# Performance work log

Hardware: AMD Instinct MI355X
Metric: run time of the kernel (lower is better)

## Reference

```python
import jax, jax.numpy as jnp
import numpy as np

TOP_K = 2
SCALING = 32.0 / 16.0  # lora_alpha / r

N, D, O = 4096, 4096, 4096   # tokens, in_features, out_features
E, H, R_RANK = 8, 3, 16      # experts, B-heads per expert, lora rank
W_SCALE = 0.02               # keep logits in a sane range


def setup_inputs() -> dict:
    key = jax.random.key(0)
    ks = jax.random.split(key, 6)
    return {
        "x": jax.random.normal(ks[0], (N, D), jnp.float32),
        "base_W": jax.random.normal(ks[1], (D, O), jnp.float32) * W_SCALE,
        "router_W": jax.random.normal(ks[2], (E, D), jnp.float32) * W_SCALE,
        "A": jax.random.normal(ks[3], (E, D, R_RANK), jnp.float32) * W_SCALE,
        "B": jax.random.normal(ks[4], (E, H, R_RANK, O), jnp.float32) * W_SCALE,
        "R": jax.random.normal(ks[5], (E, D, H), jnp.float32) * W_SCALE,
    }


def reference(x, base_W, router_W, A, B, R):
    # Base dense layer
    base = x @ base_W                                   # [N, O]
    # Expert router: softmax over experts, top-k gate renormalized
    probs = jax.nn.softmax(x @ router_W.T, axis=-1)     # [N, E]
    topv, topi = jax.lax.top_k(probs, TOP_K)            # [N, k]
    topv = topv / topv.sum(-1, keepdims=True)
    n_idx = jnp.arange(x.shape[0])[:, None]
    gate = jnp.zeros_like(probs).at[n_idx, topi].set(topv)  # dense [N, E] gate, 0 off top-k
    # Shared lora_A per expert
    a = jnp.einsum('nd,edr->ner', x, A)                 # [N, E, r]
    # Per-expert head router over lora_B heads
    head_w = jax.nn.softmax(jnp.einsum('nd,edh->neh', x, R), axis=-1)  # [N, E, H]
    # Head-weighted B projections, combined with expert gates
    delta = jnp.einsum('ner,neh,ehro,ne->no', a, head_w, B, gate)      # [N, O]
    return base + SCALING * delta
```

## Files before the change

kernel.cpp:

```cpp
#include <hip/hip_runtime.h>
#include <hip/hip_bf16.h>
#include <math.h>

typedef __bf16 bf16_t;
typedef __bf16 bf16x4_t __attribute__((ext_vector_type(4)));
typedef __bf16 bf16x8_t __attribute__((ext_vector_type(8)));
typedef float  f32x4_t  __attribute__((ext_vector_type(4)));

#define N_TOK 4096
#define D_IN  4096
#define O_OUT 4096
#define NEXP  8
#define NHEAD 3
#define RANK  16
#define KC2   384
#define PCOLS 256
#define NKZ   8
#define SCALING_F 2.0f


__device__ __forceinline__ void transpose_tile(const float* __restrict__ src,
                                               bf16_t* __restrict__ dst,
                                               int Rr, int Cc, int r0, int c0,
                                               float (*tile)[65]) {
  int q  = threadIdx.x & 15;
  int r4 = threadIdx.x >> 4;
  #pragma unroll
  for (int g = 0; g < 4; ++g) {
    int r = r4 + g * 16;
    float4 v = *(const float4*)(src + (size_t)(r0 + r) * Cc + c0 + q * 4);
    tile[r][q * 4 + 0] = v.x; tile[r][q * 4 + 1] = v.y;
    tile[r][q * 4 + 2] = v.z; tile[r][q * 4 + 3] = v.w;
  }
  __syncthreads();
  int j  = threadIdx.x & 7;
  int cc = threadIdx.x >> 3;
  #pragma unroll
  for (int h = 0; h < 2; ++h) {
    int c = cc + h * 32;
    bf16x8_t o;
    #pragma unroll
    for (int i = 0; i < 8; ++i) o[i] = (bf16_t)tile[j * 8 + i][c];
    *(bf16x8_t*)(dst + (size_t)(c0 + c) * Rr + r0 + j * 8) = o;
  }
}

__global__ __launch_bounds__(256) void prep_kernel(const float* __restrict__ x,
                                                   const float* __restrict__ base_W,
                                                   const float* __restrict__ rw,
                                                   const float* __restrict__ A,
                                                   const float* __restrict__ B,
                                                   const float* __restrict__ Rm,
                                                   bf16_t* __restrict__ xb,
                                                   bf16_t* __restrict__ WbT,
                                                   bf16_t* __restrict__ BbT,
                                                   bf16_t* __restrict__ PabT,
                                                   int* __restrict__ gidx,
                                                   float* __restrict__ gwv) {
  __shared__ float tile[64][65];
  int b = blockIdx.x;
  if (b < 4096) {
    transpose_tile(base_W, WbT, 4096, 4096, (b & 63) * 64, (b >> 6) * 64, tile);
  } else if (b < 5120) {
    int lane = threadIdx.x & 63;
    int wv = threadIdx.x >> 6;
    int n = (b - 4096) * 4 + wv;
    const float4* xv = (const float4*)(x + (size_t)n * D_IN);
    bf16x4_t* xo = (bf16x4_t*)(xb + (size_t)n * D_IN);
    float acc[NEXP] = {0, 0, 0, 0, 0, 0, 0, 0};
    for (int d = lane; d < D_IN / 4; d += 64) {
      float4 xx = xv[d];
      bf16x4_t ob = { (bf16_t)xx.x, (bf16_t)xx.y, (bf16_t)xx.z, (bf16_t)xx.w };
      xo[d] = ob;
      #pragma unroll
      for (int e = 0; e < NEXP; ++e) {
        float4 ww = ((const float4*)(rw + (size_t)e * D_IN))[d];
        acc[e] += xx.x * ww.x + xx.y * ww.y + xx.z * ww.z + xx.w * ww.w;
      }
    }
    #pragma unroll
    for (int e = 0; e < NEXP; ++e) {
      float v = acc[e];
      #pragma unroll
      for (int o = 32; o > 0; o >>= 1) v += __shfl_down(v, o);
      acc[e] = v;
    }
    if (lane == 0) {
      int i0 = 0; float l0 = acc[0];
      #pragma unroll
      for (int e = 1; e < NEXP; ++e) if (acc[e] > l0) { l0 = acc[e]; i0 = e; }
      int i1 = -1; float l1 = -3.4e38f;
      #pragma unroll
      for (int e = 0; e < NEXP; ++e) if (e != i0 && acc[e] > l1) { l1 = acc[e]; i1 = e; }
      float w0 = 1.f / (1.f + expf(l1 - l0));
      gidx[2 * n] = i0; gidx[2 * n + 1] = i1;
      gwv[2 * n] = w0;  gwv[2 * n + 1] = 1.f - w0;
    }
  } else if (b < 5504) {
    int t = b - 5120;
    transpose_tile(B, BbT, KC2, 4096, (t % 6) * 64, (t / 6) * 64, tile);
  } else {
    int c = b - 5504;
    for (int d = threadIdx.x; d < D_IN; d += 256) {
      float v = 0.f;
      if (c < 128) {
        int e = c >> 4, r = c & 15;
        v = A[((size_t)e * D_IN + d) * RANK + r];
      } else if (c < 152) {
        int qq = c - 128; int e = qq / 3, h = qq - 3 * e;
        v = Rm[((size_t)e * D_IN + d) * NHEAD + h];
      }
      PabT[(size_t)c * D_IN + d] = (bf16_t)v;
    }
  }
}

__global__ void gating_kernel(const float* __restrict__ projP, const int* __restrict__ gidx,
                              const float* __restrict__ gwv, bf16_t* __restrict__ C2b) {
  int n = blockIdx.x;
  int c = threadIdx.x;
  int e = c / 48;
  int h = (c % 48) / 16;
  int r = c & 15;
  int i0 = gidx[2 * n], i1 = gidx[2 * n + 1];
  float g = (e == i0) ? gwv[2 * n] : (e == i1) ? gwv[2 * n + 1] : 0.f;
  float val = 0.f;
  if (g != 0.f) {
    const float* p0 = projP + (size_t)n * PCOLS;
    const size_t S = (size_t)N_TOK * PCOLS;
    float h0 = 0.f, h1 = 0.f, h2 = 0.f, av = 0.f;
    #pragma unroll
    for (int z = 0; z < NKZ; ++z) {
      const float* pz = p0 + (size_t)z * S;
      h0 += pz[128 + e * 3 + 0];
      h1 += pz[128 + e * 3 + 1];
      h2 += pz[128 + e * 3 + 2];
      av += pz[e * 16 + r];
    }
    float mx = fmaxf(h0, fmaxf(h1, h2));
    float e0 = expf(h0 - mx), e1 = expf(h1 - mx), e2 = expf(h2 - mx);
    float hw = (h == 0 ? e0 : h == 1 ? e1 : e2) / (e0 + e1 + e2);
    val = SCALING_F * g * hw * av;
  }
  C2b[(size_t)n * KC2 + c] = (bf16_t)val;
}

__device__ __forceinline__ void run_kloop(f32x4_t (&acc)[4][4], bf16_t* sA, bf16_t* sB,
                                          const bf16_t* __restrict__ Ab, int lda,
                                          const bf16_t* __restrict__ Bb, int ldb, int K) {
  const int tid = threadIdx.x;
  const int lane = tid & 63;
  const int w = tid >> 6;
  const int wm = (w >> 1) * 64;
  const int wn = (w & 1) * 64;
  const int qd = lane >> 4;
  const int ln = lane & 15;
  const int sw = ln & 7;

  size_t offA[4], offB[4];
  int lo[4];
  #pragma unroll
  for (int t = 0; t < 4; ++t) {
    int c = tid + t * 256;
    int m = c >> 3, kc = (c & 7) ^ (m & 7);
    offA[t] = (size_t)m * lda + kc * 8;
    offB[t] = (size_t)m * ldb + kc * 8;
    lo[t] = c * 8;
  }
  int rowA[4], rowB[4];
  #pragma unroll
  for (int i = 0; i < 4; ++i) {
    rowA[i] = (wm + i * 16 + ln) * 64;
    rowB[i] = (wn + i * 16 + ln) * 64;
  }

  for (int k0 = 0; k0 < K; k0 += 64) {
    __syncthreads();
    #pragma unroll
    for (int t = 0; t < 4; ++t)
      __builtin_amdgcn_global_load_lds(
          (const __attribute__((address_space(1))) void*)(Ab + k0 + offA[t]),
          (__attribute__((address_space(3))) void*)(sA + lo[t]), 16, 0, 0);
    #pragma unroll
    for (int t = 0; t < 4; ++t)
      __builtin_amdgcn_global_load_lds(
          (const __attribute__((address_space(1))) void*)(Bb + k0 + offB[t]),
          (__attribute__((address_space(3))) void*)(sB + lo[t]), 16, 0, 0);
    __syncthreads();
    #pragma unroll
    for (int s = 0; s < 2; ++s) {
      bf16x8_t af[4], bfr[4];
      int kx = ((s * 4 + qd) ^ sw) * 8;
      #pragma unroll
      for (int i = 0; i < 4; ++i) af[i]  = *(const bf16x8_t*)(sA + rowA[i] + kx);
      #pragma unroll
      for (int i = 0; i < 4; ++i) bfr[i] = *(const bf16x8_t*)(sB + rowB[i] + kx);
      #pragma unroll
      for (int i = 0; i < 4; ++i)
        #pragma unroll
        for (int j = 0; j < 4; ++j)
          acc[i][j] = __builtin_amdgcn_mfma_f32_16x16x32_bf16(af[i], bfr[j], acc[i][j], 0, 0, 0);
    }
  }
}

__global__ __launch_bounds__(256) void gemm_proj_kernel(const bf16_t* __restrict__ xb,
                                                        const bf16_t* __restrict__ PabT,
                                                        float* __restrict__ projP) {
  __shared__ bf16_t sA[128 * 64];
  __shared__ bf16_t sB[128 * 64];
  int bm = blockIdx.x, bn = blockIdx.y, kz = blockIdx.z;
  f32x4_t acc[4][4] = {};
  run_kloop(acc, sA, sB,
            xb + (size_t)bm * 128 * D_IN + kz * 512, D_IN,
            PabT + (size_t)bn * 128 * D_IN + kz * 512, D_IN, 512);
  const int lane = threadIdx.x & 63, w = threadIdx.x >> 6;
  const int wm = (w >> 1) * 64, wn = (w & 1) * 64, qd = lane >> 4, ln = lane & 15;
  float* Cb = projP + (size_t)kz * N_TOK * PCOLS + (size_t)bm * 128 * PCOLS + bn * 128;
  #pragma unroll
  for (int i = 0; i < 4; ++i)
    #pragma unroll
    for (int j = 0; j < 4; ++j) {
      int col = wn + j * 16 + ln;
      #pragma unroll
      for (int rg = 0; rg < 4; ++rg) {
        int row = wm + i * 16 + qd * 4 + rg;
        Cb[(size_t)row * PCOLS + col] = acc[i][j][rg];
      }
    }
}


__device__ __forceinline__ void stage1(const bf16_t* __restrict__ G, int k0,
                                       bf16_t* lbase, size_t g, int tid) {
  __builtin_amdgcn_global_load_lds(
      (const __attribute__((address_space(1))) void*)(G + g + k0),
      (__attribute__((address_space(3))) void*)(lbase + tid * 8), 16, 0, 0);
}

template <int N>
__device__ __forceinline__ void vm_wait() {
  if constexpr (N == 6)      asm volatile("s_waitcnt vmcnt(6)" ::: "memory");
  else if constexpr (N == 4) asm volatile("s_waitcnt vmcnt(4)" ::: "memory");
  else if constexpr (N == 2) asm volatile("s_waitcnt vmcnt(2)" ::: "memory");
  else if constexpr (N == 0) asm volatile("s_waitcnt vmcnt(0)" ::: "memory");
}

template <int SC, bool STAGE, int VMN>
__device__ __forceinline__ void tbodyS(f32x4_t (&acc)[4][4], bf16_t* sring,
                                       const bf16_t* __restrict__ Ag,
                                       const bf16_t* __restrict__ Bg, int k3,
                                       size_t gA, size_t gB, int aoff, int boff, int tid) {
  constexpr int SS = (SC + 3) & 3;
  if constexpr (STAGE) {
    stage1(Ag, k3, sring + SS * 16384, gA, tid);
    stage1(Bg, k3, sring + SS * 16384 + 8192, gB, tid);
  }
  vm_wait<VMN>();
  __builtin_amdgcn_s_barrier();
  const bf16_t* pA = sring + SC * 16384 + aoff;
  const bf16_t* pB = sring + SC * 16384 + 8192 + boff;
  bf16x8_t af[4], bv[4];
  #pragma unroll
  for (int nj = 0; nj < 4; ++nj) bv[nj] = *(const bf16x8_t*)(pB + nj * 512);
  #pragma unroll
  for (int mi = 0; mi < 4; ++mi) af[mi] = *(const bf16x8_t*)(pA + mi * 512);
  __builtin_amdgcn_s_setprio(1);
  #pragma unroll
  for (int mi = 0; mi < 4; ++mi)
    #pragma unroll
    for (int nj = 0; nj < 4; ++nj)
      acc[mi][nj] = __builtin_amdgcn_mfma_f32_16x16x32_bf16(af[mi], bv[nj], acc[mi][nj], 0, 0, 0);
  __builtin_amdgcn_s_setprio(0);
  __builtin_amdgcn_sched_barrier(0);
  __builtin_amdgcn_s_barrier();
}

template <int K>
__device__ __forceinline__ void kloopS(f32x4_t (&acc)[4][4], bf16_t* sring,
                                       const bf16_t* __restrict__ A, int lda,
                                       const bf16_t* __restrict__ B, int ldb,
                                       int tid, int aoff, int boff) {
  constexpr int T = K / 32;
  static_assert((T & 3) == 0, "T must be multiple of 4");
  const int s = tid, r = s >> 2, c = (s & 3) ^ ((r >> 1) & 3);
  const size_t gA = (size_t)r * lda + c * 8;
  const size_t gB = (size_t)r * ldb + c * 8;

  #pragma unroll
  for (int t = 0; t < 3; ++t) {
    stage1(A, t * 32, sring + t * 16384, gA, tid);
    stage1(B, t * 32, sring + t * 16384 + 8192, gB, tid);
  }
  constexpr int TM = T - 3;
  int t = 0;
  for (; t + 3 < TM; t += 4) {
    tbodyS<0,true,6>(acc, sring, A, B, (t+3)*32, gA, gB, aoff, boff, tid);
    tbodyS<1,true,6>(acc, sring, A, B, (t+4)*32, gA, gB, aoff, boff, tid);
    tbodyS<2,true,6>(acc, sring, A, B, (t+5)*32, gA, gB, aoff, boff, tid);
    tbodyS<3,true,6>(acc, sring, A, B, (t+6)*32, gA, gB, aoff, boff, tid);
  }
  tbodyS<0,true,6>(acc, sring, A, B, (t+3)*32, gA, gB, aoff, boff, tid);
  tbodyS<1,false,4>(acc, sring, A, B, 0, gA, gB, aoff, boff, tid);
  tbodyS<2,false,2>(acc, sring, A, B, 0, gA, gB, aoff, boff, tid);
  tbodyS<3,false,0>(acc, sring, A, B, 0, gA, gB, aoff, boff, tid);
}

__global__ __launch_bounds__(1024, 1) void gemm_fused256(const bf16_t* __restrict__ xb,
                                                         const bf16_t* __restrict__ WbT,
                                                         const bf16_t* __restrict__ C2b,
                                                         const bf16_t* __restrict__ BbT,
                                                         float* __restrict__ out) {
  __shared__ __align__(16) bf16_t sring[4 * 16384];
  const int tid = threadIdx.x;
  const int lane = tid & 63;
  const int w = tid >> 6;
  const int wm = w >> 2;
  const int wn = w & 3;
  const int qd = lane >> 4;
  const int ln = lane & 15;
  const int swz8 = ((qd ^ ((ln >> 1) & 3)) << 3);

  int b = blockIdx.x;
  int sw = (b & 7) * 32 + (b >> 3);
  int bm = sw >> 4, bn = sw & 15;

  const int aoff = (wm * 64 + ln) * 32 + swz8;
  const int boff = (wn * 64 + ln) * 32 + swz8;

  f32x4_t acc[4][4] = {};

  kloopS<D_IN>(acc, sring, xb  + (size_t)bm * 256 * D_IN, D_IN,
                           WbT + (size_t)bn * 256 * D_IN, D_IN, tid, aoff, boff);
  kloopS<KC2>(acc, sring, C2b + (size_t)bm * 256 * KC2,  KC2,
                          BbT + (size_t)bn * 256 * KC2,  KC2,  tid, aoff, boff);

  float* Cb = out + (size_t)(bm * 256 + wm * 64) * O_OUT + bn * 256 + wn * 64;
  #pragma unroll
  for (int mi = 0; mi < 4; ++mi)
    #pragma unroll
    for (int nj = 0; nj < 4; ++nj)
      #pragma unroll
      for (int rg = 0; rg < 4; ++rg)
        Cb[(size_t)(mi * 16 + qd * 4 + rg) * O_OUT + nj * 16 + ln] = acc[mi][nj][rg];
}

extern "C" void kernel_launch(void* const* d_in, const int* in_sizes, int n_in,
                              void* d_out, int out_size, void* d_ws, size_t ws_size,
                              hipStream_t stream) {
  const float* x       = (const float*)d_in[0];
  const float* base_W  = (const float*)d_in[1];
  const float* routerW = (const float*)d_in[2];
  const float* A       = (const float*)d_in[3];
  const float* B       = (const float*)d_in[4];
  const float* Rm      = (const float*)d_in[5];
  float* out = (float*)d_out;
  char* ws = (char*)d_ws;

  bf16_t* xb   = (bf16_t*)(ws);
  bf16_t* WbT  = (bf16_t*)(ws + 33554432);
  bf16_t* PabT = (bf16_t*)(ws + 67108864);
  bf16_t* BbT  = (bf16_t*)(ws + 69206016);
  bf16_t* C2b  = (bf16_t*)(ws + 72351744);
  int*    gidx = (int*)   (ws + 75497472);
  float*  gwv  = (float*) (ws + 75530240);
  float*  projP = out;

  prep_kernel<<<5760, 256, 0, stream>>>(x, base_W, routerW, A, B, Rm,
                                        xb, WbT, BbT, PabT, gidx, gwv);
  gemm_proj_kernel<<<dim3(32, 2, NKZ), 256, 0, stream>>>(xb, PabT, projP);
  gating_kernel<<<4096, 384, 0, stream>>>(projP, gidx, gwv, C2b);
  gemm_fused256<<<dim3(256), 1024, 0, stream>>>(xb, WbT, C2b, BbT, out);
}
```

Before: 360.5 us.

## Shrink fused GEMM tile to 128x256 with double-buffered LDS and more blocks

The main fused GEMM moves from 256x256 tiles with 1024 threads and a 4-deep LDS ring to 128x256 tiles with 512 threads, a 2-stage double buffer, and 512 blocks. Launch bounds now allow several blocks per CU, so latency can be hidden across blocks instead of by deep prefetch within one block. Each thread now issues three async global-to-LDS loads per k-step. The trade is less operand reuse per tile and more global traffic for the B matrix, and the shallower prefetch could expose memory latency.

```diff
diff --git a/kernel.cpp b/kernel.cpp
--- a/kernel.cpp
+++ b/kernel.cpp
@@ -231,35 +231,39 @@
 }
 
 
-__device__ __forceinline__ void stage1(const bf16_t* __restrict__ G, int k0,
-                                       bf16_t* lbase, size_t g, int tid) {
+__device__ __forceinline__ void stageH(const bf16_t* __restrict__ Ag,
+                                       const bf16_t* __restrict__ Bg, int k0,
+                                       bf16_t* slot, size_t gA, size_t gB0, size_t gB1,
+                                       int tid) {
   __builtin_amdgcn_global_load_lds(
-      (const __attribute__((address_space(1))) void*)(G + g + k0),
-      (__attribute__((address_space(3))) void*)(lbase + tid * 8), 16, 0, 0);
+      (const __attribute__((address_space(1))) void*)(Ag + gA + k0),
+      (__attribute__((address_space(3))) void*)(slot + tid * 8), 16, 0, 0);
+  __builtin_amdgcn_global_load_lds(
+      (const __attribute__((address_space(1))) void*)(Bg + gB0 + k0),
+      (__attribute__((address_space(3))) void*)(slot + 4096 + tid * 8), 16, 0, 0);
+  __builtin_amdgcn_global_load_lds(
+      (const __attribute__((address_space(1))) void*)(Bg + gB1 + k0),
+      (__attribute__((address_space(3))) void*)(slot + 8192 + tid * 8), 16, 0, 0);
 }
 
 template <int N>
 __device__ __forceinline__ void vm_wait() {
-  if constexpr (N == 6)      asm volatile("s_waitcnt vmcnt(6)" ::: "memory");
-  else if constexpr (N == 4) asm volatile("s_waitcnt vmcnt(4)" ::: "memory");
-  else if constexpr (N == 2) asm volatile("s_waitcnt vmcnt(2)" ::: "memory");
+  if constexpr (N == 3)      asm volatile("s_waitcnt vmcnt(3)" ::: "memory");
   else if constexpr (N == 0) asm volatile("s_waitcnt vmcnt(0)" ::: "memory");
 }
 
 template <int SC, bool STAGE, int VMN>
-__device__ __forceinline__ void tbodyS(f32x4_t (&acc)[4][4], bf16_t* sring,
+__device__ __forceinline__ void tbodyH(f32x4_t (&acc)[4][4], bf16_t* sring,
                                        const bf16_t* __restrict__ Ag,
-                                       const bf16_t* __restrict__ Bg, int k3,
-                                       size_t gA, size_t gB, int aoff, int boff, int tid) {
-  constexpr int SS = (SC + 3) & 3;
-  if constexpr (STAGE) {
-    stage1(Ag, k3, sring + SS * 16384, gA, tid);
-    stage1(Bg, k3, sring + SS * 16384 + 8192, gB, tid);
-  }
+                                       const bf16_t* __restrict__ Bg, int k1,
+                                       size_t gA, size_t gB0, size_t gB1,
+                                       int aoff, int boff, int tid) {
+  if constexpr (STAGE)
+    stageH(Ag, Bg, k1, sring + (SC ^ 1) * 12288, gA, gB0, gB1, tid);
   vm_wait<VMN>();
   __builtin_amdgcn_s_barrier();
-  const bf16_t* pA = sring + SC * 16384 + aoff;
-  const bf16_t* pB = sring + SC * 16384 + 8192 + boff;
+  const bf16_t* pA = sring + SC * 12288 + aoff;
+  const bf16_t* pB = sring + SC * 12288 + 4096 + boff;
   bf16x8_t af[4], bv[4];
   #pragma unroll
   for (int nj = 0; nj < 4; ++nj) bv[nj] = *(const bf16x8_t*)(pB + nj * 512);
@@ -277,41 +281,35 @@
 }
 
 template <int K>
-__device__ __forceinline__ void kloopS(f32x4_t (&acc)[4][4], bf16_t* sring,
+__device__ __forceinline__ void kloopH(f32x4_t (&acc)[4][4], bf16_t* sring,
                                        const bf16_t* __restrict__ A, int lda,
                                        const bf16_t* __restrict__ B, int ldb,
                                        int tid, int aoff, int boff) {
   constexpr int T = K / 32;
-  static_assert((T & 3) == 0, "T must be multiple of 4");
-  const int s = tid, r = s >> 2, c = (s & 3) ^ ((r >> 1) & 3);
-  const size_t gA = (size_t)r * lda + c * 8;
-  const size_t gB = (size_t)r * ldb + c * 8;
-
-  #pragma unroll
-  for (int t = 0; t < 3; ++t) {
-    stage1(A, t * 32, sring + t * 16384, gA, tid);
-    stage1(B, t * 32, sring + t * 16384 + 8192, gB, tid);
-  }
-  constexpr int TM = T - 3;
+  static_assert((T & 1) == 0, "T must be even");
+  const int sa = tid,        ra = sa >> 2, ca = (sa & 3) ^ ((ra >> 1) & 3);
+  const int s0 = tid,        r0 = s0 >> 2, c0 = (s0 & 3) ^ ((r0 >> 1) & 3);
+  const int s1 = 512 + tid,  r1 = s1 >> 2, c1 = (s1 & 3) ^ ((r1 >> 1) & 3);
+  const size_t gA  = (size_t)ra * lda + ca * 8;
+  const size_t gB0 = (size_t)r0 * ldb + c0 * 8;
+  const size_t gB1 = (size_t)r1 * ldb + c1 * 8;
+
+  stageH(A, B, 0, sring, gA, gB0, gB1, tid);
   int t = 0;
-  for (; t + 3 < TM; t += 4) {
-    tbodyS<0,true,6>(acc, sring, A, B, (t+3)*32, gA, gB, aoff, boff, tid);
-    tbodyS<1,true,6>(acc, sring, A, B, (t+4)*32, gA, gB, aoff, boff, tid);
-    tbodyS<2,true,6>(acc, sring, A, B, (t+5)*32, gA, gB, aoff, boff, tid);
-    tbodyS<3,true,6>(acc, sring, A, B, (t+6)*32, gA, gB, aoff, boff, tid);
-  }
-  tbodyS<0,true,6>(acc, sring, A, B, (t+3)*32, gA, gB, aoff, boff, tid);
-  tbodyS<1,false,4>(acc, sring, A, B, 0, gA, gB, aoff, boff, tid);
-  tbodyS<2,false,2>(acc, sring, A, B, 0, gA, gB, aoff, boff, tid);
-  tbodyS<3,false,0>(acc, sring, A, B, 0, gA, gB, aoff, boff, tid);
-}
-
-__global__ __launch_bounds__(1024, 1) void gemm_fused256(const bf16_t* __restrict__ xb,
-                                                         const bf16_t* __restrict__ WbT,
-                                                         const bf16_t* __restrict__ C2b,
-                                                         const bf16_t* __restrict__ BbT,
-                                                         float* __restrict__ out) {
-  __shared__ __align__(16) bf16_t sring[4 * 16384];
+  for (; t + 2 < T; t += 2) {
+    tbodyH<0, true, 3>(acc, sring, A, B, (t + 1) * 32, gA, gB0, gB1, aoff, boff, tid);
+    tbodyH<1, true, 3>(acc, sring, A, B, (t + 2) * 32, gA, gB0, gB1, aoff, boff, tid);
+  }
+  tbodyH<0, true, 3>(acc, sring, A, B, (T - 1) * 32, gA, gB0, gB1, aoff, boff, tid);
+  tbodyH<1, false, 0>(acc, sring, A, B, 0, gA, gB0, gB1, aoff, boff, tid);
+}
+
+__global__ __launch_bounds__(512, 4) void gemm_fused256(const bf16_t* __restrict__ xb,
+                                                        const bf16_t* __restrict__ WbT,
+                                                        const bf16_t* __restrict__ C2b,
+                                                        const bf16_t* __restrict__ BbT,
+                                                        float* __restrict__ out) {
+  __shared__ __align__(16) bf16_t sring[2 * 12288];
   const int tid = threadIdx.x;
   const int lane = tid & 63;
   const int w = tid >> 6;
@@ -322,7 +320,7 @@
   const int swz8 = ((qd ^ ((ln >> 1) & 3)) << 3);
 
   int b = blockIdx.x;
-  int sw = (b & 7) * 32 + (b >> 3);
+  int sw = (b & 7) * 64 + (b >> 3);
   int bm = sw >> 4, bn = sw & 15;
 
   const int aoff = (wm * 64 + ln) * 32 + swz8;
@@ -330,12 +328,12 @@
 
   f32x4_t acc[4][4] = {};
 
-  kloopS<D_IN>(acc, sring, xb  + (size_t)bm * 256 * D_IN, D_IN,
+  kloopH<D_IN>(acc, sring, xb  + (size_t)bm * 128 * D_IN, D_IN,
                            WbT + (size_t)bn * 256 * D_IN, D_IN, tid, aoff, boff);
-  kloopS<KC2>(acc, sring, C2b + (size_t)bm * 256 * KC2,  KC2,
+  kloopH<KC2>(acc, sring, C2b + (size_t)bm * 128 * KC2,  KC2,
                           BbT + (size_t)bn * 256 * KC2,  KC2,  tid, aoff, boff);
 
-  float* Cb = out + (size_t)(bm * 256 + wm * 64) * O_OUT + bn * 256 + wn * 64;
+  float* Cb = out + (size_t)(bm * 128 + wm * 64) * O_OUT + bn * 256 + wn * 64;
   #pragma unroll
   for (int mi = 0; mi < 4; ++mi)
     #pragma unroll
@@ -370,5 +368,5 @@
                                         xb, WbT, BbT, PabT, gidx, gwv);
   gemm_proj_kernel<<<dim3(32, 2, NKZ), 256, 0, stream>>>(xb, PabT, projP);
   gating_kernel<<<4096, 384, 0, stream>>>(projP, gidx, gwv, C2b);
-  gemm_fused256<<<dim3(256), 1024, 0, stream>>>(xb, WbT, C2b, BbT, out);
-}
+  gemm_fused256<<<dim3(512), 512, 0, stream>>>(xb, WbT, C2b, BbT, out);
+}
```

Result: slower. 382.5 us (+6.1%).
